# Performance work log

Measured on AMD Instinct MI355X. Metric: run time of the kernel, lower is better.

The kernel has to match this reference:

```python
import jax, jax.numpy as jnp
import numpy as np

B, L, H, D, M = 4, 2048, 16, 64, 128
EPS = 1e-6


def _create_projection_matrix(key, m, d):
    nb_full_blocks = m // d
    keys = jax.random.split(key, nb_full_blocks + 2)
    blocks = []
    for i in range(nb_full_blocks):
        unstructured = jax.random.normal(keys[i], (d, d), dtype=jnp.float32)
        q, _ = jnp.linalg.qr(unstructured)
        blocks.append(q.T)
    remaining = m - nb_full_blocks * d
    if remaining > 0:
        unstructured = jax.random.normal(keys[nb_full_blocks], (d, d), dtype=jnp.float32)
        q, _ = jnp.linalg.qr(unstructured)
        blocks.append(q.T[:remaining])
    final = jnp.concatenate(blocks, axis=0)  # [m, d]
    multiplier = jnp.linalg.norm(jax.random.normal(keys[-1], (m, d), dtype=jnp.float32), axis=1)
    return multiplier[:, None] * final


def setup_inputs() -> dict:
    key = jax.random.key(0)
    kq, kk, kv, kp = jax.random.split(key, 4)
    return {
        "q": jax.random.normal(kq, (B, L, H, D), dtype=jnp.float32),
        "k": jax.random.normal(kk, (B, L, H, D), dtype=jnp.float32),
        "v": jax.random.normal(kv, (B, L, H, D), dtype=jnp.float32),
        "projection_matrix": _create_projection_matrix(kp, M, D),
    }


def _softmax_kernel(data, proj, is_query, eps=EPS):
    # data: [B,L,H,D], proj: [M,D]
    data = (data.shape[-1] ** -0.25) * data
    ratio = proj.shape[0] ** -0.5
    data_dash = jnp.einsum('blhd,md->blhm', data, proj)  # [B,L,H,M]
    diag = jnp.sum(data * data, axis=-1, keepdims=True) * 0.5  # [B,L,H,1]
    if is_query:
        mx = jnp.max(data_dash, axis=-1, keepdims=True)
    else:
        mx = jnp.max(data_dash, axis=(1, 3), keepdims=True)
    return ratio * (jnp.exp(data_dash - diag - mx) + eps)


def reference(q, k, v, projection_matrix):
    qp = _softmax_kernel(q, projection_matrix, True)   # [B,L,H,M]
    kp = _softmax_kernel(k, projection_matrix, False)  # [B,L,H,M]
    # move L to the front for the causal scan
    qs = jnp.swapaxes(qp, 0, 1)  # [L,B,H,M]
    ks = jnp.swapaxes(kp, 0, 1)  # [L,B,H,M]
    vs = jnp.swapaxes(v, 0, 1)   # [L,B,H,D]

    def step(carry, inp):
        s, dsum = carry                 # s: [B,H,M,D], dsum: [B,H,M]
        q_t, k_t, v_t = inp
        s = s + k_t[..., :, None] * v_t[..., None, :]  # outer product accumulate
        dsum = dsum + k_t
        num = jnp.einsum('bhmd,bhm->bhd', s, q_t)      # [B,H,D]
        den = jnp.einsum('bhm,bhm->bh', q_t, dsum)     # [B,H]
        return (s, dsum), (num, den)

    init = (jnp.zeros((qs.shape[1], qs.shape[2], qs.shape[3], vs.shape[3]), qs.dtype),
            jnp.zeros_like(ks[0]))
    _, (nums, dens) = jax.lax.scan(step, init, (qs, ks, vs))
    av = jnp.swapaxes(nums, 0, 1)          # [B,L,H,D]
    norm = jnp.swapaxes(dens, 0, 1)[..., None]  # [B,L,H,1]
    return av / norm
```

## Files before the change

### kernel.cpp

```cpp
#include <hip/hip_runtime.h>
#include <math.h>

#define B_ 4
#define L_ 2048
#define H_ 16
#define D_ 64
#define M_ 128
#define TC_ 64
#define NC_ (L_ / TC_)
#define EPSK 1e-6f
#define DATA_SCALE 0.35355339059327379f
#define RATIO 0.08838834764831845f

typedef __bf16 bf16;
typedef bf16 bf16x4 __attribute__((ext_vector_type(4)));
typedef bf16 bf16x8 __attribute__((ext_vector_type(8)));
typedef float floatx4 __attribute__((ext_vector_type(4)));

#define PK128 136
#define PK64 72

__device__ __forceinline__ unsigned pk(bf16 a, bf16 b) {
    return (unsigned)__builtin_bit_cast(unsigned short, a) |
           ((unsigned)__builtin_bit_cast(unsigned short, b) << 16);
}
__device__ __forceinline__ void split2(float x, bf16& hi, bf16& lo) {
    hi = (bf16)x;
    lo = (bf16)(x - (float)hi);
}

__device__ __forceinline__ unsigned enc_f(float f) {
    unsigned u = __float_as_uint(f);
    return (u & 0x80000000u) ? ~u : (u | 0x80000000u);
}
__device__ __forceinline__ float dec_f(unsigned u) {
    unsigned b = (u & 0x80000000u) ? (u ^ 0x80000000u) : ~u;
    return __uint_as_float(b);
}

__global__ void init_mx(unsigned* __restrict__ mx) {
    if (threadIdx.x < B_ * H_) mx[threadIdx.x] = 0u;
}

template <int MODE>
__global__ __launch_bounds__(256) void feat_mfma(const float* __restrict__ data,
                                                 const float* __restrict__ proj,
                                                 unsigned* __restrict__ mxk,
                                                 bf16* __restrict__ outp,
                                                 bf16* __restrict__ outT) {
    __shared__ __align__(16) bf16 ahi[64 * PK64], alo[64 * PK64];
    __shared__ __align__(16) bf16 phi[128 * PK64], plo[128 * PK64];
    __shared__ __align__(16) bf16 sc[64 * 130];
    __shared__ float diag_s[64];
    __shared__ float wred[4];

    int tid = threadIdx.x;
    int blk = blockIdx.x;
    int c = blk & 31, h = (blk >> 5) & 15, b = blk >> 9;
    int l0 = c * 64;

    const float4* p4 = (const float4*)proj;
#pragma unroll
    for (int i = 0; i < 8; i++) {
        int ch = tid + 256 * i;
        int m = ch >> 4, c4 = ch & 15;
        float4 x = p4[ch];
        bf16 h0, h1, h2, h3, l0_, l1, l2, l3;
        split2(x.x, h0, l0_); split2(x.y, h1, l1);
        split2(x.z, h2, l2);  split2(x.w, h3, l3);
        uint2 uh = {pk(h0, h1), pk(h2, h3)};
        uint2 ul = {pk(l0_, l1), pk(l2, l3)};
        *(uint2*)&phi[m * PK64 + c4 * 4] = uh;
        *(uint2*)&plo[m * PK64 + c4 * 4] = ul;
    }
#pragma unroll
    for (int i = 0; i < 4; i++) {
        int ch = tid + 256 * i;
        int row = ch >> 4, c4 = ch & 15;
        const float4* gp = (const float4*)(data +
            ((size_t)(b * L_ + l0 + row) * H_ + h) * D_) + c4;
        float4 x = *gp;
        float a0 = DATA_SCALE * x.x, a1 = DATA_SCALE * x.y;
        float a2 = DATA_SCALE * x.z, a3 = DATA_SCALE * x.w;
        bf16 h0, h1, h2, h3, l0_, l1, l2, l3;
        split2(a0, h0, l0_); split2(a1, h1, l1);
        split2(a2, h2, l2);  split2(a3, h3, l3);
        uint2 uh = {pk(h0, h1), pk(h2, h3)};
        uint2 ul = {pk(l0_, l1), pk(l2, l3)};
        *(uint2*)&ahi[row * PK64 + c4 * 4] = uh;
        *(uint2*)&alo[row * PK64 + c4 * 4] = ul;
        if (MODE != 0) {
            float ss = a0 * a0 + a1 * a1 + a2 * a2 + a3 * a3;
            ss += __shfl_xor(ss, 1, 64);
            ss += __shfl_xor(ss, 2, 64);
            ss += __shfl_xor(ss, 4, 64);
            ss += __shfl_xor(ss, 8, 64);
            if ((tid & 15) == 0) diag_s[row] = 0.5f * ss;
        }
    }
    __syncthreads();

    int w = tid >> 6, lane = tid & 63, lr = lane & 15, quad = lane >> 4;
    const bf16* abh = ahi + (16 * w + lr) * PK64 + quad * 8;
    const bf16* abl = alo + (16 * w + lr) * PK64 + quad * 8;

    floatx4 acc[8];
#pragma unroll
    for (int tc = 0; tc < 8; tc++) acc[tc] = (floatx4){0.f, 0.f, 0.f, 0.f};

#pragma unroll
    for (int k0 = 0; k0 < 64; k0 += 32) {
        bf16x8 ah = *(const bf16x8*)(abh + k0);
        bf16x8 al = *(const bf16x8*)(abl + k0);
#pragma unroll
        for (int tc = 0; tc < 8; tc++) {
            bf16x8 bh = *(const bf16x8*)(phi + (16 * tc + lr) * PK64 + quad * 8 + k0);
            bf16x8 bl = *(const bf16x8*)(plo + (16 * tc + lr) * PK64 + quad * 8 + k0);
            acc[tc] = __builtin_amdgcn_mfma_f32_16x16x32_bf16(ah, bh, acc[tc], 0, 0, 0);
            acc[tc] = __builtin_amdgcn_mfma_f32_16x16x32_bf16(al, bh, acc[tc], 0, 0, 0);
            acc[tc] = __builtin_amdgcn_mfma_f32_16x16x32_bf16(ah, bl, acc[tc], 0, 0, 0);
        }
    }

    if (MODE == 0) {
        float mm = acc[0][0];
#pragma unroll
        for (int tc = 0; tc < 8; tc++)
#pragma unroll
            for (int reg = 0; reg < 4; reg++) mm = fmaxf(mm, acc[tc][reg]);
#pragma unroll
        for (int off = 1; off < 64; off <<= 1) mm = fmaxf(mm, __shfl_xor(mm, off, 64));
        if (lane == 0) wred[w] = mm;
        __syncthreads();
        if (tid == 0) {
            float g = fmaxf(fmaxf(wred[0], wred[1]), fmaxf(wred[2], wred[3]));
            atomicMax(&mxk[b * H_ + h], enc_f(g));
        }
        return;
    }

    int t0 = 16 * w + 4 * quad;
    float mxg = 0.f;
    if (MODE == 1) mxg = dec_f(mxk[b * H_ + h]);

    float rm[4];
    if (MODE == 2) {
#pragma unroll
        for (int reg = 0; reg < 4; reg++) {
            float m = acc[0][reg];
#pragma unroll
            for (int tc = 1; tc < 8; tc++) m = fmaxf(m, acc[tc][reg]);
            m = fmaxf(m, __shfl_xor(m, 1, 64));
            m = fmaxf(m, __shfl_xor(m, 2, 64));
            m = fmaxf(m, __shfl_xor(m, 4, 64));
            m = fmaxf(m, __shfl_xor(m, 8, 64));
            rm[reg] = m;
        }
    }

#pragma unroll
    for (int reg = 0; reg < 4; reg++) {
        float dg = diag_s[t0 + reg];
        float sh = (MODE == 1) ? (dg + mxg) : (dg + rm[reg]);
#pragma unroll
        for (int tc = 0; tc < 8; tc++) {
            float val = RATIO * (expf(acc[tc][reg] - sh) + EPSK);
            sc[(t0 + reg) * 130 + 16 * tc + lr] = (bf16)val;
        }
    }
    __syncthreads();

#pragma unroll
    for (int i = 0; i < 16; i++) {
        int e = tid + 256 * i;
        int row = e >> 6, mp = e & 63;
        unsigned u = pk(sc[row * 130 + 2 * mp], sc[row * 130 + 2 * mp + 1]);
        *(unsigned*)(outp + ((size_t)(b * L_ + l0 + row) * H_ + h) * M_ + 2 * mp) = u;
    }
    if (MODE == 1) {
#pragma unroll
        for (int i = 0; i < 16; i++) {
            int e = tid + 256 * i;
            int m = e >> 5, t2 = (e & 31) * 2;
            unsigned u = pk(sc[t2 * 130 + m], sc[(t2 + 1) * 130 + m]);
            *(unsigned*)(outT + ((size_t)(b * H_ + h) * M_ + m) * L_ + l0 + t2) = u;
        }
    }
}

__global__ __launch_bounds__(256) void v_tr(const float* __restrict__ v,
                                            bf16* __restrict__ vbT) {
    __shared__ __align__(16) bf16 vt[64 * 66];
    int tid = threadIdx.x;
    int blk = blockIdx.x;
    int c = blk & 31, hh = (blk >> 5) & 15, b = blk >> 9;
#pragma unroll
    for (int i = 0; i < 4; i++) {
        int ch = tid + 256 * i;
        int row = ch >> 4, c4 = ch & 15;
        size_t gb = ((size_t)(b * L_ + c * 64 + row) * H_ + hh) * D_;
        float4 x = *(const float4*)(v + gb + c4 * 4);
        unsigned* lp = (unsigned*)(vt + row * 66 + c4 * 4);
        lp[0] = pk((bf16)x.x, (bf16)x.y);
        lp[1] = pk((bf16)x.z, (bf16)x.w);
    }
    __syncthreads();
    size_t ob = (size_t)((b * H_ + hh) * D_) * (size_t)L_ + c * 64;
#pragma unroll
    for (int i = 0; i < 8; i++) {
        int e2 = tid + 256 * i;
        int d = e2 >> 5, tau2 = (e2 & 31) * 2;
        *(unsigned*)(vbT + ob + (size_t)d * L_ + tau2) =
            pk(vt[tau2 * 66 + d], vt[(tau2 + 1) * 66 + d]);
    }
}

__global__ __launch_bounds__(256) void chunk_mfma(const bf16* __restrict__ kpT,
                                                  const bf16* __restrict__ vbT,
                                                  bf16* __restrict__ S,
                                                  float* __restrict__ ds) {
    __shared__ __align__(16) bf16 kT[128 * PK64];
    __shared__ __align__(16) bf16 vT[64 * PK64];
    int tid = threadIdx.x;
    int blk = blockIdx.x;
    int c = blk & 31, bh = blk >> 5;
    int l0 = c * 64;
#pragma unroll
    for (int i = 0; i < 4; i++) {
        int ch = tid + 256 * i;
        int m = ch >> 3, c8 = ch & 7;
        *(uint4*)(kT + m * PK64 + c8 * 8) =
            ((const uint4*)kpT)[(((size_t)bh * M_ + m) * L_ + l0) / 8 + c8];
    }
#pragma unroll
    for (int i = 0; i < 2; i++) {
        int ch = tid + 256 * i;
        int d = ch >> 3, c8 = ch & 7;
        *(uint4*)(vT + d * PK64 + c8 * 8) =
            ((const uint4*)vbT)[(((size_t)bh * D_ + d) * L_ + l0) / 8 + c8];
    }
    __syncthreads();

    int w = tid >> 6, lane = tid & 63, lr = lane & 15, quad = lane >> 4;
    floatx4 acc[8];
#pragma unroll
    for (int tc = 0; tc < 8; tc++) acc[tc] = (floatx4){0.f, 0.f, 0.f, 0.f};
#pragma unroll
    for (int k0 = 0; k0 < 64; k0 += 32) {
        bf16x8 a = *(const bf16x8*)(vT + (16 * w + lr) * PK64 + k0 + quad * 8);
#pragma unroll
        for (int tc = 0; tc < 8; tc++) {
            bf16x8 bb = *(const bf16x8*)(kT + (16 * tc + lr) * PK64 + k0 + quad * 8);
            acc[tc] = __builtin_amdgcn_mfma_f32_16x16x32_bf16(a, bb, acc[tc], 0, 0, 0);
        }
    }

    float dsv = 0.f;
    {
        int m = tid >> 1, half = tid & 1;
        const bf16x8* kr = (const bf16x8*)(kT + m * PK64 + half * 32);
#pragma unroll
        for (int j = 0; j < 4; j++) {
            bf16x8 vv = kr[j];
#pragma unroll
            for (int e = 0; e < 8; e++) dsv += (float)vv[e];
        }
        dsv += __shfl_xor(dsv, 1, 64);
    }
    __syncthreads();

    bf16* scr = kT;
    int d0 = 16 * w + 4 * quad;
#pragma unroll
    for (int tc = 0; tc < 8; tc++)
#pragma unroll
        for (int reg = 0; reg < 4; reg++)
            scr[(d0 + reg) * 128 + 16 * tc + lr] = (bf16)acc[tc][reg];
    if ((tid & 1) == 0) ds[(size_t)blk * M_ + (tid >> 1)] = dsv;
    __syncthreads();
#pragma unroll
    for (int i = 0; i < 4; i++) {
        int e = tid + 256 * i;
        ((uint4*)S)[(size_t)blk * 1024 + e] = ((const uint4*)scr)[e];
    }
}

__global__ void prefix_S(unsigned* __restrict__ S) {
    int blk = blockIdx.x;
    int seg = blk & 15, bh = blk >> 4;
    int p = seg * 256 + threadIdx.x;
    size_t base = (size_t)bh * NC_ * 4096 + p;
    float c0 = 0.f, c1 = 0.f;
    for (int c = 0; c < NC_; c++) {
        size_t a = base + (size_t)c * 4096;
        unsigned u = S[a];
        float f0 = (float)__builtin_bit_cast(bf16, (unsigned short)(u & 0xffffu));
        float f1 = (float)__builtin_bit_cast(bf16, (unsigned short)(u >> 16));
        S[a] = pk((bf16)c0, (bf16)c1);
        c0 += f0; c1 += f1;
    }
}

__global__ void prefix_D(float* __restrict__ ds) {
    int bh = blockIdx.x;
    int m = threadIdx.x;
    size_t base = (size_t)bh * NC_ * M_ + m;
    float carry = 0.f;
    for (int c = 0; c < NC_; c++) {
        size_t a = base + (size_t)c * M_;
        float val = ds[a];
        ds[a] = carry;
        carry += val;
    }
}

__global__ __launch_bounds__(256) void attn_mfma(const bf16* __restrict__ qp,
                                                 const bf16* __restrict__ kp,
                                                 const bf16* __restrict__ vbT,
                                                 const bf16* __restrict__ Sp,
                                                 const float* __restrict__ dp,
                                                 float* __restrict__ out) {
    __shared__ __align__(16) bf16 arena[64 * PK128 * 2 + 64 * PK64];
    bf16* ks  = arena;
    bf16* spT = arena + 64 * PK128;
    bf16* sc  = spT;
    bf16* vT  = arena + 2 * 64 * PK128;
    __shared__ float dprevL[128];
    __shared__ float den0_l[64];
    __shared__ float densc_l[64];

    int tid = threadIdx.x;
    int blk = blockIdx.x;
    int c = blk & 31, bh = blk >> 5;
    int h = bh & 15, b = bh >> 4;
    int l0 = c * 64;

#pragma unroll
    for (int i = 0; i < 4; i++) {
        int ch = tid + 256 * i;
        int row = ch >> 4, c8 = ch & 15;
        size_t gb = (((size_t)(b * L_ + l0 + row) * H_ + h) * M_) / 8;
        *(uint4*)(ks + row * PK128 + c8 * 8) = ((const uint4*)kp)[gb + c8];
    }
#pragma unroll
    for (int i = 0; i < 4; i++) {
        int ch = tid + 256 * i;
        int row = ch >> 4, c8 = ch & 15;
        *(uint4*)(spT + row * PK128 + c8 * 8) = ((const uint4*)Sp)[(size_t)blk * 1024 + ch];
    }
#pragma unroll
    for (int i = 0; i < 2; i++) {
        int ch = tid + 256 * i;
        int d = ch >> 3, c8 = ch & 7;
        *(uint4*)(vT + d * PK64 + c8 * 8) =
            ((const uint4*)vbT)[(((size_t)bh * D_ + d) * L_ + l0) / 8 + c8];
    }
    if (tid < 128) dprevL[tid] = dp[(size_t)blk * M_ + tid];
    __syncthreads();

    {
        int t = tid >> 2, p = tid & 3;
        const bf16* qrow = qp + ((size_t)(b * L_ + l0 + t) * H_ + h) * M_ + p * 32;
        float s = 0.f;
#pragma unroll
        for (int j = 0; j < 4; j++) {
            bf16x8 vv = *(const bf16x8*)(qrow + 8 * j);
#pragma unroll
            for (int e = 0; e < 8; e++) s += (float)vv[e] * dprevL[p * 32 + 8 * j + e];
        }
        s += __shfl_xor(s, 1, 64);
        s += __shfl_xor(s, 2, 64);
        if (p == 0) den0_l[t] = s;
    }

    int w = tid >> 6, lane = tid & 63, lr = lane & 15, quad = lane >> 4;

    bf16x8 af[4];
    {
        const bf16* qb = qp + ((size_t)(b * L_ + l0 + 16 * w + lr) * H_ + h) * M_ + quad * 8;
#pragma unroll
        for (int k = 0; k < 4; k++) af[k] = *(const bf16x8*)(qb + 32 * k);
    }

    floatx4 acc[4];
#pragma unroll
    for (int tc = 0; tc < 4; tc++) acc[tc] = (floatx4){0.f, 0.f, 0.f, 0.f};

#pragma unroll
    for (int ki = 0; ki < 4; ki++) {
#pragma unroll
        for (int tc = 0; tc < 4; tc++) {
            bf16x8 bb = *(const bf16x8*)(spT + (16 * tc + lr) * PK128 + 32 * ki + quad * 8);
            acc[tc] = __builtin_amdgcn_mfma_f32_16x16x32_bf16(af[ki], bb, acc[tc], 0, 0, 0);
        }
    }

    floatx4 acc2[4];
#pragma unroll
    for (int tc = 0; tc < 4; tc++) acc2[tc] = (floatx4){0.f, 0.f, 0.f, 0.f};
#pragma unroll
    for (int ki = 0; ki < 4; ki++) {
        for (int tc = 0; tc <= w; tc++) {
            bf16x8 bb = *(const bf16x8*)(ks + (16 * tc + lr) * PK128 + 32 * ki + quad * 8);
            acc2[tc] = __builtin_amdgcn_mfma_f32_16x16x32_bf16(af[ki], bb, acc2[tc], 0, 0, 0);
        }
    }
    __syncthreads();

    {
        float dsum[4] = {0.f, 0.f, 0.f, 0.f};
        int t0 = 16 * w + 4 * quad;
#pragma unroll
        for (int tc = 0; tc < 4; tc++) {
#pragma unroll
            for (int reg = 0; reg < 4; reg++) {
                int tg = t0 + reg, tau = 16 * tc + lr;
                float vv = (tc <= w) ? acc2[tc][reg] : 0.f;
                if (tau > tg) vv = 0.f;
                dsum[reg] += vv;
                sc[tg * PK64 + tau] = (bf16)vv;
            }
        }
#pragma unroll
        for (int reg = 0; reg < 4; reg++) {
            float s = dsum[reg];
            s += __shfl_xor(s, 1, 64);
            s += __shfl_xor(s, 2, 64);
            s += __shfl_xor(s, 4, 64);
            s += __shfl_xor(s, 8, 64);
            if (lr == 0) densc_l[t0 + reg] = s;
        }
    }
    __syncthreads();

    {
        int kmax = (w >= 2) ? 64 : 32;
        for (int k0 = 0; k0 < kmax; k0 += 32) {
            bf16x8 a = *(const bf16x8*)(sc + (16 * w + lr) * PK64 + k0 + quad * 8);
#pragma unroll
            for (int tc = 0; tc < 4; tc++) {
                bf16x8 bb = *(const bf16x8*)(vT + (16 * tc + lr) * PK64 + k0 + quad * 8);
                acc[tc] = __builtin_amdgcn_mfma_f32_16x16x32_bf16(a, bb, acc[tc], 0, 0, 0);
            }
        }
    }

    {
        int t0 = 16 * w + 4 * quad;
        float inv[4];
#pragma unroll
        for (int reg = 0; reg < 4; reg++)
            inv[reg] = 1.0f / (den0_l[t0 + reg] + densc_l[t0 + reg]);
#pragma unroll
        for (int tc = 0; tc < 4; tc++)
#pragma unroll
            for (int reg = 0; reg < 4; reg++)
                out[((size_t)(b * L_ + l0 + t0 + reg) * H_ + h) * D_ + 16 * tc + lr] =
                    acc[tc][reg] * inv[reg];
    }
}

extern "C" void kernel_launch(void* const* d_in, const int* in_sizes, int n_in,
                              void* d_out, int out_size, void* d_ws, size_t ws_size,
                              hipStream_t stream) {
    const float* q = (const float*)d_in[0];
    const float* k = (const float*)d_in[1];
    const float* v = (const float*)d_in[2];
    const float* proj = (const float*)d_in[3];
    float* out = (float*)d_out;
    char* W = (char*)d_ws;

    bf16* qp   = (bf16*)(W);
    bf16* kp   = (bf16*)(W + 33554432ull);
    bf16* kpT  = (bf16*)(W + 67108864ull);
    bf16* vbT  = (bf16*)(W + 100663296ull);
    bf16* S    = (bf16*)(W + 117440512ull);
    float* ds  = (float*)(W + 150994944ull);
    unsigned* mx = (unsigned*)(W + 152043520ull);

    hipLaunchKernelGGL(init_mx, dim3(1), dim3(64), 0, stream, mx);
    hipLaunchKernelGGL((feat_mfma<0>), dim3(2048), dim3(256), 0, stream,
                       k, proj, mx, (bf16*)nullptr, (bf16*)nullptr);
    hipLaunchKernelGGL((feat_mfma<1>), dim3(2048), dim3(256), 0, stream,
                       k, proj, mx, kp, kpT);
    hipLaunchKernelGGL((feat_mfma<2>), dim3(2048), dim3(256), 0, stream,
                       q, proj, mx, qp, (bf16*)nullptr);
    hipLaunchKernelGGL(v_tr, dim3(2048), dim3(256), 0, stream, v, vbT);
    hipLaunchKernelGGL(chunk_mfma, dim3(2048), dim3(256), 0, stream, kpT, vbT, S, ds);
    hipLaunchKernelGGL(prefix_S, dim3(1024), dim3(256), 0, stream, (unsigned*)S);
    hipLaunchKernelGGL(prefix_D, dim3(64), dim3(128), 0, stream, ds);
    hipLaunchKernelGGL(attn_mfma, dim3(2048), dim3(256), 0, stream,
                       qp, kp, vbT, S, ds, out);
}
```

Measured before the change: 275.7 us.

## Pre-split projection into MFMA fragment layout once and load operands directly into registers

Adds a small kernel that splits the projection matrix into bf16 hi/lo parts once, stored in per-lane MFMA fragment order, so feature kernels load B operands straight from global memory instead of re-splitting the matrix into LDS in each of 2048 blocks. Data rows are loaded directly into registers and the diag is computed with cross-lane shuffles, removing the LDS staging and a barrier. The max-only pass (MODE 0) now uses a single bf16 MFMA without the hi/lo correction terms, and expf is replaced with __expf. Together these cut setup work and LDS traffic, but the lower-precision max pass and the fast exp can slightly change the global key max and the numerics.

```diff
diff --git a/kernel.cpp b/kernel.cpp
--- a/kernel.cpp
+++ b/kernel.cpp
@@ -38,87 +38,87 @@
     return __uint_as_float(b);
 }
 
-__global__ void init_mx(unsigned* __restrict__ mx) {
-    if (threadIdx.x < B_ * H_) mx[threadIdx.x] = 0u;
+__global__ __launch_bounds__(256) void proj_split(const float* __restrict__ proj,
+                                                  bf16* __restrict__ pfh,
+                                                  bf16* __restrict__ pfl,
+                                                  unsigned* __restrict__ mx) {
+    int f = blockIdx.x * 256 + threadIdx.x;
+    if (blockIdx.x == 0 && threadIdx.x < B_ * H_) mx[threadIdx.x] = 0u;
+    int tc = f >> 7, k0h = (f >> 6) & 1, lane = f & 63;
+    int lr = lane & 15, quad = lane >> 4;
+    const float* src = proj + (16 * tc + lr) * 64 + k0h * 32 + quad * 8;
+    float4 x0 = *(const float4*)src;
+    float4 x1 = *(const float4*)(src + 4);
+    float a[8] = {x0.x, x0.y, x0.z, x0.w, x1.x, x1.y, x1.z, x1.w};
+    bf16x8 hi, lo;
+#pragma unroll
+    for (int e = 0; e < 8; e++) {
+        bf16 h = (bf16)a[e];
+        hi[e] = h;
+        lo[e] = (bf16)(a[e] - (float)h);
+    }
+    *(bf16x8*)(pfh + (size_t)f * 8) = hi;
+    *(bf16x8*)(pfl + (size_t)f * 8) = lo;
 }
 
 template <int MODE>
 __global__ __launch_bounds__(256) void feat_mfma(const float* __restrict__ data,
-                                                 const float* __restrict__ proj,
+                                                 const bf16* __restrict__ pfh,
+                                                 const bf16* __restrict__ pfl,
                                                  unsigned* __restrict__ mxk,
                                                  bf16* __restrict__ outp,
                                                  bf16* __restrict__ outT) {
-    __shared__ __align__(16) bf16 ahi[64 * PK64], alo[64 * PK64];
-    __shared__ __align__(16) bf16 phi[128 * PK64], plo[128 * PK64];
     __shared__ __align__(16) bf16 sc[64 * 130];
-    __shared__ float diag_s[64];
     __shared__ float wred[4];
 
     int tid = threadIdx.x;
     int blk = blockIdx.x;
     int c = blk & 31, h = (blk >> 5) & 15, b = blk >> 9;
     int l0 = c * 64;
-
-    const float4* p4 = (const float4*)proj;
-#pragma unroll
-    for (int i = 0; i < 8; i++) {
-        int ch = tid + 256 * i;
-        int m = ch >> 4, c4 = ch & 15;
-        float4 x = p4[ch];
-        bf16 h0, h1, h2, h3, l0_, l1, l2, l3;
-        split2(x.x, h0, l0_); split2(x.y, h1, l1);
-        split2(x.z, h2, l2);  split2(x.w, h3, l3);
-        uint2 uh = {pk(h0, h1), pk(h2, h3)};
-        uint2 ul = {pk(l0_, l1), pk(l2, l3)};
-        *(uint2*)&phi[m * PK64 + c4 * 4] = uh;
-        *(uint2*)&plo[m * PK64 + c4 * 4] = ul;
-    }
-#pragma unroll
-    for (int i = 0; i < 4; i++) {
-        int ch = tid + 256 * i;
-        int row = ch >> 4, c4 = ch & 15;
-        const float4* gp = (const float4*)(data +
-            ((size_t)(b * L_ + l0 + row) * H_ + h) * D_) + c4;
-        float4 x = *gp;
-        float a0 = DATA_SCALE * x.x, a1 = DATA_SCALE * x.y;
-        float a2 = DATA_SCALE * x.z, a3 = DATA_SCALE * x.w;
-        bf16 h0, h1, h2, h3, l0_, l1, l2, l3;
-        split2(a0, h0, l0_); split2(a1, h1, l1);
-        split2(a2, h2, l2);  split2(a3, h3, l3);
-        uint2 uh = {pk(h0, h1), pk(h2, h3)};
-        uint2 ul = {pk(l0_, l1), pk(l2, l3)};
-        *(uint2*)&ahi[row * PK64 + c4 * 4] = uh;
-        *(uint2*)&alo[row * PK64 + c4 * 4] = ul;
-        if (MODE != 0) {
-            float ss = a0 * a0 + a1 * a1 + a2 * a2 + a3 * a3;
-            ss += __shfl_xor(ss, 1, 64);
-            ss += __shfl_xor(ss, 2, 64);
-            ss += __shfl_xor(ss, 4, 64);
-            ss += __shfl_xor(ss, 8, 64);
-            if ((tid & 15) == 0) diag_s[row] = 0.5f * ss;
-        }
-    }
-    __syncthreads();
-
     int w = tid >> 6, lane = tid & 63, lr = lane & 15, quad = lane >> 4;
-    const bf16* abh = ahi + (16 * w + lr) * PK64 + quad * 8;
-    const bf16* abl = alo + (16 * w + lr) * PK64 + quad * 8;
+
+    const float* drow = data +
+        ((size_t)(b * L_ + l0 + 16 * w + lr) * H_ + h) * D_ + quad * 8;
+    bf16x8 ah[2], al[2];
+    float ss = 0.f;
+#pragma unroll
+    for (int k0 = 0; k0 < 2; k0++) {
+        float4 x0 = *(const float4*)(drow + k0 * 32);
+        float4 x1 = *(const float4*)(drow + k0 * 32 + 4);
+        float a[8] = {x0.x, x0.y, x0.z, x0.w, x1.x, x1.y, x1.z, x1.w};
+#pragma unroll
+        for (int e = 0; e < 8; e++) {
+            float s = DATA_SCALE * a[e];
+            if (MODE != 0) ss += s * s;
+            bf16 hh = (bf16)s;
+            ah[k0][e] = hh;
+            if (MODE != 0) al[k0][e] = (bf16)(s - (float)hh);
+        }
+    }
+    float ssrow = 0.f;
+    if (MODE != 0) {
+        ss += __shfl_xor(ss, 16, 64);
+        ss += __shfl_xor(ss, 32, 64);
+        ssrow = 0.5f * ss;
+    }
 
     floatx4 acc[8];
 #pragma unroll
     for (int tc = 0; tc < 8; tc++) acc[tc] = (floatx4){0.f, 0.f, 0.f, 0.f};
 
-#pragma unroll
-    for (int k0 = 0; k0 < 64; k0 += 32) {
-        bf16x8 ah = *(const bf16x8*)(abh + k0);
-        bf16x8 al = *(const bf16x8*)(abl + k0);
-#pragma unroll
-        for (int tc = 0; tc < 8; tc++) {
-            bf16x8 bh = *(const bf16x8*)(phi + (16 * tc + lr) * PK64 + quad * 8 + k0);
-            bf16x8 bl = *(const bf16x8*)(plo + (16 * tc + lr) * PK64 + quad * 8 + k0);
-            acc[tc] = __builtin_amdgcn_mfma_f32_16x16x32_bf16(ah, bh, acc[tc], 0, 0, 0);
-            acc[tc] = __builtin_amdgcn_mfma_f32_16x16x32_bf16(al, bh, acc[tc], 0, 0, 0);
-            acc[tc] = __builtin_amdgcn_mfma_f32_16x16x32_bf16(ah, bl, acc[tc], 0, 0, 0);
+    const bf16x8* ph = (const bf16x8*)pfh + lane;
+    const bf16x8* pl = (const bf16x8*)pfl + lane;
+#pragma unroll
+    for (int tc = 0; tc < 8; tc++) {
+#pragma unroll
+        for (int k0 = 0; k0 < 2; k0++) {
+            bf16x8 bh = ph[(tc * 2 + k0) * 64];
+            acc[tc] = __builtin_amdgcn_mfma_f32_16x16x32_bf16(ah[k0], bh, acc[tc], 0, 0, 0);
+            if (MODE != 0) {
+                bf16x8 bl = pl[(tc * 2 + k0) * 64];
+                acc[tc] = __builtin_amdgcn_mfma_f32_16x16x32_bf16(al[k0], bh, acc[tc], 0, 0, 0);
+                acc[tc] = __builtin_amdgcn_mfma_f32_16x16x32_bf16(ah[k0], bl, acc[tc], 0, 0, 0);
+            }
         }
     }
 
@@ -160,11 +160,11 @@
 
 #pragma unroll
     for (int reg = 0; reg < 4; reg++) {
-        float dg = diag_s[t0 + reg];
+        float dg = __shfl(ssrow, 4 * quad + reg, 64);
         float sh = (MODE == 1) ? (dg + mxg) : (dg + rm[reg]);
 #pragma unroll
         for (int tc = 0; tc < 8; tc++) {
-            float val = RATIO * (expf(acc[tc][reg] - sh) + EPSK);
+            float val = RATIO * (__expf(acc[tc][reg] - sh) + EPSK);
             sc[(t0 + reg) * 130 + 16 * tc + lr] = (bf16)val;
         }
     }
@@ -477,14 +477,16 @@
     bf16* S    = (bf16*)(W + 117440512ull);
     float* ds  = (float*)(W + 150994944ull);
     unsigned* mx = (unsigned*)(W + 152043520ull);
-
-    hipLaunchKernelGGL(init_mx, dim3(1), dim3(64), 0, stream, mx);
+    bf16* pfh  = (bf16*)(W + 152043776ull);
+    bf16* pfl  = (bf16*)(W + 152060160ull);
+
+    hipLaunchKernelGGL(proj_split, dim3(4), dim3(256), 0, stream, proj, pfh, pfl, mx);
     hipLaunchKernelGGL((feat_mfma<0>), dim3(2048), dim3(256), 0, stream,
-                       k, proj, mx, (bf16*)nullptr, (bf16*)nullptr);
+                       k, pfh, pfl, mx, (bf16*)nullptr, (bf16*)nullptr);
     hipLaunchKernelGGL((feat_mfma<1>), dim3(2048), dim3(256), 0, stream,
-                       k, proj, mx, kp, kpT);
+                       k, pfh, pfl, mx, kp, kpT);
     hipLaunchKernelGGL((feat_mfma<2>), dim3(2048), dim3(256), 0, stream,
-                       q, proj, mx, qp, (bf16*)nullptr);
+                       q, pfh, pfl, mx, qp, (bf16*)nullptr);
     hipLaunchKernelGGL(v_tr, dim3(2048), dim3(256), 0, stream, v, vbT);
     hipLaunchKernelGGL(chunk_mfma, dim3(2048), dim3(256), 0, stream, kpT, vbT, S, ds);
     hipLaunchKernelGGL(prefix_S, dim3(1024), dim3(256), 0, stream, (unsigned*)S);
```

Measured after the change: 247.9 us. 10.1% less time.
